# Performance work log

Measured on AMD Instinct MI355X. Metric: run time of the kernel, lower is better.

## Reference

```python
import jax, jax.numpy as jnp
import numpy as np

HEAD_NUM = 6

def setup_inputs() -> dict:
    key = jax.random.key(0)
    k1, k2, k3 = jax.random.split(key, 3)
    B, N, P, C = 4, 64, 256, 384
    x = jax.random.normal(k1, (B, N, P, C), dtype=jnp.float32)
    # torch Linear init scale ~ 1/sqrt(fan_in); keep magnitudes sane
    w_qkv = jax.random.normal(k2, (C, 3 * C), dtype=jnp.float32) * (1.0 / np.sqrt(C))
    w_proj = jax.random.normal(k3, (C, C), dtype=jnp.float32) * (1.0 / np.sqrt(C))
    b_proj = jnp.zeros((C,), dtype=jnp.float32)
    return {"x": x, "w_qkv": w_qkv, "w_proj": w_proj, "b_proj": b_proj}

def reference(x, w_qkv, w_proj, b_proj):
    B, N, P, C = x.shape
    H = HEAD_NUM
    D = C // H
    scale = jnp.asarray(D, dtype=x.dtype)  # NOTE: head_dim ** 1, faithful to source
    qkv = (x @ w_qkv).reshape(B, N, P, 3, H, D)
    q = qkv[:, :, :, 0]  # (B, N, P, H, D)
    k = qkv[:, :, :, 1]
    v = qkv[:, :, :, 2]
    attn = jnp.einsum('bnphd,bnqhd->bnhpq', q, k) * scale  # (B,N,H,P,P)
    attn = jax.nn.softmax(attn, axis=-1)
    out = jnp.einsum('bnhpq,bnqhd->bnphd', attn, v).reshape(B, N, P, C)
    return out @ w_proj + b_proj
```

## Files before the change

kernel.cpp:

```cpp
#include <hip/hip_runtime.h>

typedef __bf16 bf16_t;
typedef __bf16 bf16x8 __attribute__((ext_vector_type(8)));
typedef float f32x4 __attribute__((ext_vector_type(4)));
typedef unsigned short u16;
typedef unsigned short u16x4 __attribute__((ext_vector_type(4)));
typedef unsigned int u32;

#define B_ 4
#define N_ 64
#define P_ 256
#define C_ 384
#define H_ 6
#define D_ 64
#define M_TOTAL 65536
#define NQKV 1152
#define KSTEPS 12
#define NFRAG 12
#define WF_HSTRIDE (KSTEPS*NFRAG*512)
#define FUSED_LDS 131072
#define NBLK (H_*B_*N_)

__device__ __forceinline__ u16 f2b(float f){ return __builtin_bit_cast(u16, (bf16_t)f); }
__device__ __forceinline__ f32x4 mfma(bf16x8 a, bf16x8 b, f32x4 c){
    return __builtin_amdgcn_mfma_f32_16x16x32_bf16(a, b, c, 0, 0, 0);
}

__global__ __launch_bounds__(256) void prep_w(
    const float* __restrict__ wqkv, const float* __restrict__ wproj,
    u16* __restrict__ Wfh, u16* __restrict__ Wfl, u16* __restrict__ wPt)
{
    int i = blockIdx.x * 256 + threadIdx.x;
    const int NSLOT = H_ * KSTEPS * NFRAG * 64;
    if (i < NSLOT) {
        int lane = i & 63;
        int frag = i >> 6;
        int nf = frag % NFRAG;
        int ks = (frag / NFRAG) % KSTEPS;
        int h  = frag / (NFRAG * KSTEPS);
        int part = nf >> 2;
        int nh   = (nf & 3) * 16 + (lane & 15);
        int col  = part * C_ + h * 64 + nh;
        int k0   = ks * 32 + (lane >> 4) * 8;
        #pragma unroll
        for (int e = 0; e < 8; ++e) {
            float w = wqkv[(size_t)(k0 + e) * NQKV + col];
            bf16_t hi = (bf16_t)w;
            Wfh[(size_t)i * 8 + e] = __builtin_bit_cast(u16, hi);
            Wfl[(size_t)i * 8 + e] = f2b(w - (float)hi);
        }
    }
    int j = i - NSLOT;
    if (j >= 0 && j < C_ * C_) {
        int k = j / C_, n = j % C_;
        wPt[(size_t)n * C_ + k] = f2b(wproj[j]);
    }
}

__global__ __launch_bounds__(512)
__attribute__((amdgpu_waves_per_eu(2, 2)))
void fused_attn(
    const float* __restrict__ x, const u16* __restrict__ Wfh,
    const u16* __restrict__ Wfl, u16* __restrict__ attn)
{
    extern __shared__ u16 sm[];
    u16* Kh = sm;
    u16* Kl = sm + 16384;
    u16* Vt = sm + 32768;
    u16* Qb = sm + 49152;

    const int tid  = threadIdx.x;
    const int lane = tid & 63, wid = tid >> 6;
    const int g = lane >> 4, r16 = lane & 15;

    const int p = blockIdx.x;
    const int logical = (p & 7) * (NBLK / 8) + (p >> 3);
    const int h  = logical % H_;
    const int bn = logical / H_;
    const size_t row0 = (size_t)bn * P_;
    const int m0w = wid * 32;

    f32x4 acc[2][12];
    #pragma unroll
    for (int mf = 0; mf < 2; ++mf)
        #pragma unroll
        for (int nf = 0; nf < 12; ++nf) acc[mf][nf] = f32x4{0.f,0.f,0.f,0.f};

    const float* xr0 = x + (row0 + m0w + r16) * C_;
    const float* xr1 = xr0 + 16 * C_;
    const u16* wh = Wfh + (size_t)h * WF_HSTRIDE + lane * 8;
    const u16* wl = Wfl + (size_t)h * WF_HSTRIDE + lane * 8;

    #pragma unroll
    for (int ks = 0; ks < KSTEPS; ++ks) {
        const u16* whk = wh + ks * (NFRAG * 512);
        const u16* wlk = wl + ks * (NFRAG * 512);
        bf16x8 bh[12], bl[8];
        #pragma unroll
        for (int nf = 0; nf < 12; ++nf) bh[nf] = *(const bf16x8*)(whk + nf * 512);
        #pragma unroll
        for (int nf = 0; nf < 8; ++nf)  bl[nf] = *(const bf16x8*)(wlk + nf * 512);

        const float* xp0 = xr0 + ks * 32 + 8 * g;
        const float* xp1 = xr1 + ks * 32 + 8 * g;
        f32x4 a0 = *(const f32x4*)xp0, b0 = *(const f32x4*)(xp0 + 4);
        f32x4 a1 = *(const f32x4*)xp1, b1 = *(const f32x4*)(xp1 + 4);

        bf16x8 ah[2], al[2];
        #pragma unroll
        for (int e = 0; e < 4; ++e) {
            bf16_t h0 = (bf16_t)a0[e], h1 = (bf16_t)b0[e];
            ah[0][e] = h0;   al[0][e]   = (bf16_t)(a0[e] - (float)h0);
            ah[0][4+e] = h1; al[0][4+e] = (bf16_t)(b0[e] - (float)h1);
            bf16_t h2 = (bf16_t)a1[e], h3 = (bf16_t)b1[e];
            ah[1][e] = h2;   al[1][e]   = (bf16_t)(a1[e] - (float)h2);
            ah[1][4+e] = h3; al[1][4+e] = (bf16_t)(b1[e] - (float)h3);
        }

        #pragma unroll
        for (int nf = 0; nf < 8; ++nf) {
            acc[0][nf] = mfma(ah[0], bh[nf], acc[0][nf]);
            acc[1][nf] = mfma(ah[1], bh[nf], acc[1][nf]);
            acc[0][nf] = mfma(ah[0], bl[nf], acc[0][nf]);
            acc[1][nf] = mfma(ah[1], bl[nf], acc[1][nf]);
            acc[0][nf] = mfma(al[0], bh[nf], acc[0][nf]);
            acc[1][nf] = mfma(al[1], bh[nf], acc[1][nf]);
        }
        #pragma unroll
        for (int nf = 8; nf < 12; ++nf) {
            acc[0][nf] = mfma(ah[0], bh[nf], acc[0][nf]);
            acc[1][nf] = mfma(ah[1], bh[nf], acc[1][nf]);
        }
    }

    #pragma unroll
    for (int mf = 0; mf < 2; ++mf)
    #pragma unroll
    for (int f = 0; f < 4; ++f)
    #pragma unroll
    for (int rr = 0; rr < 4; ++rr) {
        int q = m0w + mf * 16 + 4 * g + rr;
        int d = f * 16 + r16;
        int ek = q * 64 + (((d >> 3) ^ (q & 7)) << 3) + (d & 7);
        float kv = acc[mf][4 + f][rr];
        bf16_t khi = (bf16_t)kv;
        Kh[ek] = __builtin_bit_cast(u16, khi);
        Kl[ek] = f2b(kv - (float)khi);
        Vt[d * 256 + (((q >> 3) ^ (d & 7)) << 3) + (q & 7)] = f2b(acc[mf][8 + f][rr]);
    }

    u16* myQb = Qb + wid * 2048;
    bf16x8 aqh[2][2], aql[2][2];
    #pragma unroll
    for (int mf = 0; mf < 2; ++mf)
    #pragma unroll
    for (int f = 0; f < 4; ++f)
    #pragma unroll
    for (int rr = 0; rr < 4; ++rr) {
        int r = mf * 16 + 4 * g + rr;
        int c = f * 16 + r16;
        myQb[r * 64 + (((c >> 3) ^ (r & 7)) << 3) + (c & 7)] = f2b(acc[mf][f][rr]);
    }
    #pragma unroll
    for (int mf = 0; mf < 2; ++mf)
    #pragma unroll
    for (int k2 = 0; k2 < 2; ++k2) {
        int r = mf * 16 + r16;
        aqh[mf][k2] = *(const bf16x8*)&myQb[r * 64 + (((k2 * 4 + g) ^ (r & 7)) << 3)];
    }
    __builtin_amdgcn_sched_barrier(0);
    #pragma unroll
    for (int mf = 0; mf < 2; ++mf)
    #pragma unroll
    for (int f = 0; f < 4; ++f)
    #pragma unroll
    for (int rr = 0; rr < 4; ++rr) {
        int r = mf * 16 + 4 * g + rr;
        int c = f * 16 + r16;
        float v = acc[mf][f][rr];
        bf16_t hi = (bf16_t)v;
        myQb[r * 64 + (((c >> 3) ^ (r & 7)) << 3) + (c & 7)] = f2b(v - (float)hi);
    }
    #pragma unroll
    for (int mf = 0; mf < 2; ++mf)
    #pragma unroll
    for (int k2 = 0; k2 < 2; ++k2) {
        int r = mf * 16 + r16;
        aql[mf][k2] = *(const bf16x8*)&myQb[r * 64 + (((k2 * 4 + g) ^ (r & 7)) << 3)];
    }

    __syncthreads();

    f32x4 S[2][16];
    #pragma unroll
    for (int mf = 0; mf < 2; ++mf)
        #pragma unroll
        for (int nf = 0; nf < 16; ++nf) S[mf][nf] = f32x4{0.f,0.f,0.f,0.f};

    #pragma unroll
    for (int nf = 0; nf < 16; ++nf) {
        int q = nf * 16 + r16;
        bf16x8 kh[2], kl[2];
        #pragma unroll
        for (int k2 = 0; k2 < 2; ++k2) {
            int e = q * 64 + (((k2 * 4 + g) ^ (q & 7)) << 3);
            kh[k2] = *(const bf16x8*)&Kh[e];
            kl[k2] = *(const bf16x8*)&Kl[e];
        }
        #pragma unroll
        for (int k2 = 0; k2 < 2; ++k2) {
            S[0][nf] = mfma(aqh[0][k2], kh[k2], S[0][nf]);
            S[1][nf] = mfma(aqh[1][k2], kh[k2], S[1][nf]);
            S[0][nf] = mfma(aqh[0][k2], kl[k2], S[0][nf]);
            S[1][nf] = mfma(aqh[1][k2], kl[k2], S[1][nf]);
            S[0][nf] = mfma(aql[0][k2], kh[k2], S[0][nf]);
            S[1][nf] = mfma(aql[1][k2], kh[k2], S[1][nf]);
        }
    }

    float inv_[2][4];
    #pragma unroll
    for (int mf = 0; mf < 2; ++mf) {
        float mrow[4] = {-1e30f,-1e30f,-1e30f,-1e30f};
        #pragma unroll
        for (int nf = 0; nf < 16; ++nf)
            #pragma unroll
            for (int rr = 0; rr < 4; ++rr) mrow[rr] = fmaxf(mrow[rr], S[mf][nf][rr]);
        #pragma unroll
        for (int mask = 1; mask < 16; mask <<= 1)
            #pragma unroll
            for (int rr = 0; rr < 4; ++rr) mrow[rr] = fmaxf(mrow[rr], __shfl_xor(mrow[rr], mask, 64));
        float ssum[4] = {0.f,0.f,0.f,0.f};
        #pragma unroll
        for (int nf = 0; nf < 16; ++nf)
            #pragma unroll
            for (int rr = 0; rr < 4; ++rr) {
                float pv = __expf((S[mf][nf][rr] - mrow[rr]) * 64.0f);
                S[mf][nf][rr] = pv;
                ssum[rr] += pv;
            }
        #pragma unroll
        for (int mask = 1; mask < 16; mask <<= 1)
            #pragma unroll
            for (int rr = 0; rr < 4; ++rr) ssum[rr] += __shfl_xor(ssum[rr], mask, 64);
        #pragma unroll
        for (int rr = 0; rr < 4; ++rr) inv_[mf][rr] = 1.0f / ssum[rr];
    }

    f32x4 O[2][4];
    #pragma unroll
    for (int mf = 0; mf < 2; ++mf)
        #pragma unroll
        for (int f = 0; f < 4; ++f) O[mf][f] = f32x4{0.f,0.f,0.f,0.f};

    #pragma unroll
    for (int t = 0; t < 8; ++t) {
        bf16x8 bv[4];
        #pragma unroll
        for (int f = 0; f < 4; ++f) {
            int d = f * 16 + r16;
            bv[f] = *(const bf16x8*)&Vt[d * 256 + ((((t * 32 + 8 * g) >> 3) ^ (d & 7)) << 3)];
        }
        u16* pb = myQb + (t & 1) * 1024;
        #pragma unroll
        for (int mf = 0; mf < 2; ++mf)
        #pragma unroll
        for (int tt = 0; tt < 2; ++tt) {
            int nf = 2 * t + tt;
            #pragma unroll
            for (int rr = 0; rr < 4; ++rr)
                pb[(mf * 16 + 4 * g + rr) * 32 + tt * 16 + r16] = f2b(S[mf][nf][rr] * inv_[mf][rr]);
        }
        bf16x8 ap0 = *(const bf16x8*)&pb[(r16) * 32 + 8 * g];
        bf16x8 ap1 = *(const bf16x8*)&pb[(16 + r16) * 32 + 8 * g];
        #pragma unroll
        for (int f = 0; f < 4; ++f) {
            O[0][f] = mfma(ap0, bv[f], O[0][f]);
            O[1][f] = mfma(ap1, bv[f], O[1][f]);
        }
    }

    #pragma unroll
    for (int mf = 0; mf < 2; ++mf)
    #pragma unroll
    for (int f = 0; f < 4; ++f)
    #pragma unroll
    for (int rr = 0; rr < 4; ++rr)
        attn[(row0 + m0w + mf * 16 + 4 * g + rr) * C_ + h * 64 + f * 16 + r16] = f2b(O[mf][f][rr]);
}

__global__ __launch_bounds__(256, 2) void proj_kernel(
    const u16* __restrict__ attn, const u16* __restrict__ wPt,
    const float* __restrict__ bias, float* __restrict__ out)
{
    __shared__ alignas(16) u16 As[128*32];
    __shared__ alignas(16) u16 Bs[128*32];

    const int tid = threadIdx.x;
    const int lane = tid & 63, wid = tid >> 6;
    const int wr = wid >> 1, wc = wid & 1;
    const int g = lane >> 4, r16 = lane & 15;
    const int m0 = blockIdx.x * 128;
    const int n0 = blockIdx.y * 128;

    f32x4 acc[4][4];
    for (int i = 0; i < 4; i++) for (int j = 0; j < 4; j++) acc[i][j] = f32x4{0.f,0.f,0.f,0.f};

    for (int kt = 0; kt < C_; kt += 32) {
        for (int r = 0; r < 4; ++r) {
            int i = tid + 256*r;
            int mm = i >> 3;
            int kk = (i & 7) << 2;
            u16x4 v = *(const u16x4*)&attn[(size_t)(m0+mm)*C_ + kt + kk];
            int e = mm*32 + (((kk>>3) ^ ((mm>>1)&3))<<3) + (kk&7);
            *(u16x4*)&As[e] = v;
        }
        for (int r = 0; r < 4; ++r) {
            int i = tid + 256*r;
            int nn = i >> 3;
            int kk = (i & 7) << 2;
            u16x4 v = *(const u16x4*)&wPt[(size_t)(n0+nn)*C_ + kt + kk];
            int e = nn*32 + (((kk>>3) ^ ((nn>>1)&3))<<3) + (kk&7);
            *(u16x4*)&Bs[e] = v;
        }
        __syncthreads();

        bf16x8 a[4], b[4];
        for (int i = 0; i < 4; i++) {
            int row = wr*64 + i*16 + r16;
            a[i] = *(const bf16x8*)&As[row*32 + ((g ^ ((row>>1)&3))<<3)];
        }
        for (int j = 0; j < 4; j++) {
            int n = wc*64 + j*16 + r16;
            b[j] = *(const bf16x8*)&Bs[n*32 + ((g ^ ((n>>1)&3))<<3)];
        }
        for (int i = 0; i < 4; i++) for (int j = 0; j < 4; j++)
            acc[i][j] = mfma(a[i], b[j], acc[i][j]);
        __syncthreads();
    }

    for (int i = 0; i < 4; i++) for (int j = 0; j < 4; j++) for (int rr = 0; rr < 4; rr++) {
        size_t row = m0 + wr*64 + i*16 + g*4 + rr;
        int col = n0 + wc*64 + j*16 + r16;
        out[row*C_ + col] = acc[i][j][rr] + bias[col];
    }
}

extern "C" void kernel_launch(void* const* d_in, const int* in_sizes, int n_in,
                              void* d_out, int out_size, void* d_ws, size_t ws_size,
                              hipStream_t stream)
{
    const float* x      = (const float*)d_in[0];
    const float* w_qkv  = (const float*)d_in[1];
    const float* w_proj = (const float*)d_in[2];
    const float* b_proj = (const float*)d_in[3];
    float* out = (float*)d_out;

    u16* ws = (u16*)d_ws;
    u16* attnb = ws;
    size_t off = (size_t)M_TOTAL * C_;
    u16* Wfh = ws + off; off += (size_t)H_ * WF_HSTRIDE;
    u16* Wfl = ws + off; off += (size_t)H_ * WF_HSTRIDE;
    u16* wPt = ws + off; off += (size_t)C_ * C_;

    hipFuncSetAttribute((const void*)fused_attn,
                        hipFuncAttributeMaxDynamicSharedMemorySize, FUSED_LDS);

    int prep_n = H_ * KSTEPS * NFRAG * 64 + C_ * C_;
    prep_w<<<dim3((prep_n + 255) / 256), 256, 0, stream>>>(w_qkv, w_proj, Wfh, Wfl, wPt);
    fused_attn<<<dim3(NBLK), 512, FUSED_LDS, stream>>>(x, Wfh, Wfl, attnb);
    proj_kernel<<<dim3(M_TOTAL / 128, C_ / 128), 256, 0, stream>>>(attnb, wPt, b_proj, out);
}
```

Before: 282.3 us.

## Software-pipeline weight/x loads, K and V fragment reads, pad P buffer stride

Double-buffers the QKV projection's weight and x loads across k-steps, interleaving the next step's global loads between MFMA groups with sched_barriers. It also prefetches K and V fragments from LDS one iteration ahead in the QK^T and PV loops, raising wave priority around the MFMA bursts. The P staging buffer row stride is padded from 32 to 40 to cut LDS bank conflicts, which grows the LDS footprint. Double buffering raises register pressure, which may cause spills or lower occupancy.

```diff
diff --git a/kernel.cpp b/kernel.cpp
--- a/kernel.cpp
+++ b/kernel.cpp
@@ -18,8 +18,10 @@
 #define KSTEPS 12
 #define NFRAG 12
 #define WF_HSTRIDE (KSTEPS*NFRAG*512)
-#define FUSED_LDS 131072
 #define NBLK (H_*B_*N_)
+#define FUSED_LDS 139264
+#define PB_STRIDE 40
+#define SB() __builtin_amdgcn_sched_barrier(0)
 
 __device__ __forceinline__ u16 f2b(float f){ return __builtin_bit_cast(u16, (bf16_t)f); }
 __device__ __forceinline__ f32x4 mfma(bf16x8 a, bf16x8 b, f32x4 c){
@@ -91,46 +93,92 @@
     const u16* wh = Wfh + (size_t)h * WF_HSTRIDE + lane * 8;
     const u16* wl = Wfl + (size_t)h * WF_HSTRIDE + lane * 8;
 
+    bf16x8 bhv[2][12];
+    bf16x8 blv[2][8];
+    bf16x8 ahq[2][2], alq[2][2];
+    f32x4 xr[4];
+
+#define SPLIT_A(par) do {                                                    \
+    _Pragma("unroll")                                                        \
+    for (int e = 0; e < 4; ++e) {                                            \
+        bf16_t h0 = (bf16_t)xr[0][e], h1 = (bf16_t)xr[1][e];                 \
+        ahq[par][0][e]   = h0; alq[par][0][e]   = (bf16_t)(xr[0][e] - (float)h0); \
+        ahq[par][0][4+e] = h1; alq[par][0][4+e] = (bf16_t)(xr[1][e] - (float)h1); \
+        bf16_t h2 = (bf16_t)xr[2][e], h3 = (bf16_t)xr[3][e];                 \
+        ahq[par][1][e]   = h2; alq[par][1][e]   = (bf16_t)(xr[2][e] - (float)h2); \
+        ahq[par][1][4+e] = h3; alq[par][1][4+e] = (bf16_t)(xr[3][e] - (float)h3); \
+    } } while (0)
+
+#define XLOAD(ks_) do {                                                      \
+    const float* _xp0 = xr0 + (ks_) * 32 + 8 * g;                            \
+    const float* _xp1 = xr1 + (ks_) * 32 + 8 * g;                            \
+    xr[0] = *(const f32x4*)_xp0; xr[1] = *(const f32x4*)(_xp0 + 4);          \
+    xr[2] = *(const f32x4*)_xp1; xr[3] = *(const f32x4*)(_xp1 + 4);          \
+    } while (0)
+
+    XLOAD(0);
+    {
+        const u16* whk = wh;  const u16* wlk = wl;
+        #pragma unroll
+        for (int nf = 0; nf < 12; ++nf) bhv[0][nf] = *(const bf16x8*)(whk + nf * 512);
+        #pragma unroll
+        for (int nf = 0; nf < 8;  ++nf) blv[0][nf] = *(const bf16x8*)(wlk + nf * 512);
+    }
+    SPLIT_A(0);
+
     #pragma unroll
     for (int ks = 0; ks < KSTEPS; ++ks) {
-        const u16* whk = wh + ks * (NFRAG * 512);
-        const u16* wlk = wl + ks * (NFRAG * 512);
-        bf16x8 bh[12], bl[8];
-        #pragma unroll
-        for (int nf = 0; nf < 12; ++nf) bh[nf] = *(const bf16x8*)(whk + nf * 512);
-        #pragma unroll
-        for (int nf = 0; nf < 8; ++nf)  bl[nf] = *(const bf16x8*)(wlk + nf * 512);
-
-        const float* xp0 = xr0 + ks * 32 + 8 * g;
-        const float* xp1 = xr1 + ks * 32 + 8 * g;
-        f32x4 a0 = *(const f32x4*)xp0, b0 = *(const f32x4*)(xp0 + 4);
-        f32x4 a1 = *(const f32x4*)xp1, b1 = *(const f32x4*)(xp1 + 4);
-
-        bf16x8 ah[2], al[2];
-        #pragma unroll
-        for (int e = 0; e < 4; ++e) {
-            bf16_t h0 = (bf16_t)a0[e], h1 = (bf16_t)b0[e];
-            ah[0][e] = h0;   al[0][e]   = (bf16_t)(a0[e] - (float)h0);
-            ah[0][4+e] = h1; al[0][4+e] = (bf16_t)(b0[e] - (float)h1);
-            bf16_t h2 = (bf16_t)a1[e], h3 = (bf16_t)b1[e];
-            ah[1][e] = h2;   al[1][e]   = (bf16_t)(a1[e] - (float)h2);
-            ah[1][4+e] = h3; al[1][4+e] = (bf16_t)(b1[e] - (float)h3);
-        }
-
-        #pragma unroll
-        for (int nf = 0; nf < 8; ++nf) {
-            acc[0][nf] = mfma(ah[0], bh[nf], acc[0][nf]);
-            acc[1][nf] = mfma(ah[1], bh[nf], acc[1][nf]);
-            acc[0][nf] = mfma(ah[0], bl[nf], acc[0][nf]);
-            acc[1][nf] = mfma(ah[1], bl[nf], acc[1][nf]);
-            acc[0][nf] = mfma(al[0], bh[nf], acc[0][nf]);
-            acc[1][nf] = mfma(al[1], bh[nf], acc[1][nf]);
-        }
+        const int par = ks & 1, nxt = par ^ 1;
+        const u16* whk1 = wh + (ks + 1) * (NFRAG * 512);
+        const u16* wlk1 = wl + (ks + 1) * (NFRAG * 512);
+
+        if (ks < KSTEPS - 1) {
+            XLOAD(ks + 1);
+            #pragma unroll
+            for (int nf = 0; nf < 4; ++nf) bhv[nxt][nf] = *(const bf16x8*)(whk1 + nf * 512);
+        }
+        SB();
+        #pragma unroll
+        for (int nf = 0; nf < 4; ++nf) {
+            acc[0][nf] = mfma(ahq[par][0], bhv[par][nf], acc[0][nf]);
+            acc[1][nf] = mfma(ahq[par][1], bhv[par][nf], acc[1][nf]);
+            acc[0][nf] = mfma(ahq[par][0], blv[par][nf], acc[0][nf]);
+            acc[1][nf] = mfma(ahq[par][1], blv[par][nf], acc[1][nf]);
+            acc[0][nf] = mfma(alq[par][0], bhv[par][nf], acc[0][nf]);
+            acc[1][nf] = mfma(alq[par][1], bhv[par][nf], acc[1][nf]);
+        }
+        SB();
+        if (ks < KSTEPS - 1) {
+            #pragma unroll
+            for (int nf = 0; nf < 4; ++nf) blv[nxt][nf] = *(const bf16x8*)(wlk1 + nf * 512);
+            #pragma unroll
+            for (int nf = 4; nf < 8; ++nf) bhv[nxt][nf] = *(const bf16x8*)(whk1 + nf * 512);
+        }
+        SB();
+        #pragma unroll
+        for (int nf = 4; nf < 8; ++nf) {
+            acc[0][nf] = mfma(ahq[par][0], bhv[par][nf], acc[0][nf]);
+            acc[1][nf] = mfma(ahq[par][1], bhv[par][nf], acc[1][nf]);
+            acc[0][nf] = mfma(ahq[par][0], blv[par][nf], acc[0][nf]);
+            acc[1][nf] = mfma(ahq[par][1], blv[par][nf], acc[1][nf]);
+            acc[0][nf] = mfma(alq[par][0], bhv[par][nf], acc[0][nf]);
+            acc[1][nf] = mfma(alq[par][1], bhv[par][nf], acc[1][nf]);
+        }
+        SB();
+        if (ks < KSTEPS - 1) {
+            #pragma unroll
+            for (int nf = 4; nf < 8;  ++nf) blv[nxt][nf] = *(const bf16x8*)(wlk1 + nf * 512);
+            #pragma unroll
+            for (int nf = 8; nf < 12; ++nf) bhv[nxt][nf] = *(const bf16x8*)(whk1 + nf * 512);
+            SPLIT_A(nxt);
+        }
+        SB();
         #pragma unroll
         for (int nf = 8; nf < 12; ++nf) {
-            acc[0][nf] = mfma(ah[0], bh[nf], acc[0][nf]);
-            acc[1][nf] = mfma(ah[1], bh[nf], acc[1][nf]);
-        }
+            acc[0][nf] = mfma(ahq[par][0], bhv[par][nf], acc[0][nf]);
+            acc[1][nf] = mfma(ahq[par][1], bhv[par][nf], acc[1][nf]);
+        }
+        SB();
     }
 
     #pragma unroll
@@ -149,7 +197,7 @@
         Vt[d * 256 + (((q >> 3) ^ (d & 7)) << 3) + (q & 7)] = f2b(acc[mf][8 + f][rr]);
     }
 
-    u16* myQb = Qb + wid * 2048;
+    u16* myQb = Qb + wid * 2560;
     bf16x8 aqh[2][2], aql[2][2];
     #pragma unroll
     for (int mf = 0; mf < 2; ++mf)
@@ -168,7 +216,7 @@
         int r = mf * 16 + r16;
         aqh[mf][k2] = *(const bf16x8*)&myQb[r * 64 + (((k2 * 4 + g) ^ (r & 7)) << 3)];
     }
-    __builtin_amdgcn_sched_barrier(0);
+    SB();
     #pragma unroll
     for (int mf = 0; mf < 2; ++mf)
     #pragma unroll
@@ -197,25 +245,41 @@
         #pragma unroll
         for (int nf = 0; nf < 16; ++nf) S[mf][nf] = f32x4{0.f,0.f,0.f,0.f};
 
-    #pragma unroll
-    for (int nf = 0; nf < 16; ++nf) {
-        int q = nf * 16 + r16;
-        bf16x8 kh[2], kl[2];
+    bf16x8 khv[2][2], klv[2][2];
+    {
+        int q = r16;
         #pragma unroll
         for (int k2 = 0; k2 < 2; ++k2) {
             int e = q * 64 + (((k2 * 4 + g) ^ (q & 7)) << 3);
-            kh[k2] = *(const bf16x8*)&Kh[e];
-            kl[k2] = *(const bf16x8*)&Kl[e];
-        }
+            khv[0][k2] = *(const bf16x8*)&Kh[e];
+            klv[0][k2] = *(const bf16x8*)&Kl[e];
+        }
+    }
+    #pragma unroll
+    for (int nf = 0; nf < 16; ++nf) {
+        const int par = nf & 1, nxt = par ^ 1;
+        if (nf < 15) {
+            int q = (nf + 1) * 16 + r16;
+            #pragma unroll
+            for (int k2 = 0; k2 < 2; ++k2) {
+                int e = q * 64 + (((k2 * 4 + g) ^ (q & 7)) << 3);
+                khv[nxt][k2] = *(const bf16x8*)&Kh[e];
+                klv[nxt][k2] = *(const bf16x8*)&Kl[e];
+            }
+        }
+        SB();
+        __builtin_amdgcn_s_setprio(1);
         #pragma unroll
         for (int k2 = 0; k2 < 2; ++k2) {
-            S[0][nf] = mfma(aqh[0][k2], kh[k2], S[0][nf]);
-            S[1][nf] = mfma(aqh[1][k2], kh[k2], S[1][nf]);
-            S[0][nf] = mfma(aqh[0][k2], kl[k2], S[0][nf]);
-            S[1][nf] = mfma(aqh[1][k2], kl[k2], S[1][nf]);
-            S[0][nf] = mfma(aql[0][k2], kh[k2], S[0][nf]);
-            S[1][nf] = mfma(aql[1][k2], kh[k2], S[1][nf]);
-        }
+            S[0][nf] = mfma(aqh[0][k2], khv[par][k2], S[0][nf]);
+            S[1][nf] = mfma(aqh[1][k2], khv[par][k2], S[1][nf]);
+            S[0][nf] = mfma(aqh[0][k2], klv[par][k2], S[0][nf]);
+            S[1][nf] = mfma(aqh[1][k2], klv[par][k2], S[1][nf]);
+            S[0][nf] = mfma(aql[0][k2], khv[par][k2], S[0][nf]);
+            S[1][nf] = mfma(aql[1][k2], khv[par][k2], S[1][nf]);
+        }
+        __builtin_amdgcn_s_setprio(0);
+        SB();
     }
 
     float inv_[2][4];
@@ -253,15 +317,23 @@
         #pragma unroll
         for (int f = 0; f < 4; ++f) O[mf][f] = f32x4{0.f,0.f,0.f,0.f};
 
+    bf16x8 bvv[2][4];
+    #pragma unroll
+    for (int f = 0; f < 4; ++f) {
+        int d = f * 16 + r16;
+        bvv[0][f] = *(const bf16x8*)&Vt[d * 256 + ((((8 * g) >> 3) ^ (d & 7)) << 3)];
+    }
     #pragma unroll
     for (int t = 0; t < 8; ++t) {
-        bf16x8 bv[4];
-        #pragma unroll
-        for (int f = 0; f < 4; ++f) {
-            int d = f * 16 + r16;
-            bv[f] = *(const bf16x8*)&Vt[d * 256 + ((((t * 32 + 8 * g) >> 3) ^ (d & 7)) << 3)];
-        }
-        u16* pb = myQb + (t & 1) * 1024;
+        const int par = t & 1, nxt = par ^ 1;
+        if (t < 7) {
+            #pragma unroll
+            for (int f = 0; f < 4; ++f) {
+                int d = f * 16 + r16;
+                bvv[nxt][f] = *(const bf16x8*)&Vt[d * 256 + (((((t + 1) * 32 + 8 * g) >> 3) ^ (d & 7)) << 3)];
+            }
+        }
+        u16* pb = myQb + par * 1280;
         #pragma unroll
         for (int mf = 0; mf < 2; ++mf)
         #pragma unroll
@@ -269,15 +341,17 @@
             int nf = 2 * t + tt;
             #pragma unroll
             for (int rr = 0; rr < 4; ++rr)
-                pb[(mf * 16 + 4 * g + rr) * 32 + tt * 16 + r16] = f2b(S[mf][nf][rr] * inv_[mf][rr]);
-        }
-        bf16x8 ap0 = *(const bf16x8*)&pb[(r16) * 32 + 8 * g];
-        bf16x8 ap1 = *(const bf16x8*)&pb[(16 + r16) * 32 + 8 * g];
+                pb[(mf * 16 + 4 * g + rr) * PB_STRIDE + tt * 16 + r16] = f2b(S[mf][nf][rr] * inv_[mf][rr]);
+        }
+        bf16x8 ap0 = *(const bf16x8*)&pb[(r16) * PB_STRIDE + 8 * g];
+        bf16x8 ap1 = *(const bf16x8*)&pb[(16 + r16) * PB_STRIDE + 8 * g];
+        __builtin_amdgcn_s_setprio(1);
         #pragma unroll
         for (int f = 0; f < 4; ++f) {
-            O[0][f] = mfma(ap0, bv[f], O[0][f]);
-            O[1][f] = mfma(ap1, bv[f], O[1][f]);
-        }
+            O[0][f] = mfma(ap0, bvv[par][f], O[0][f]);
+            O[1][f] = mfma(ap1, bvv[par][f], O[1][f]);
+        }
+        __builtin_amdgcn_s_setprio(0);
     }
 
     #pragma unroll
```

New measurement: 281.3 us. About the same (-0.4%).
